# Kernel tuning notes

Hardware: AMD Instinct MI355X
Metric: run time of the kernel (lower is better)

Reference implementation:

```python
import jax, jax.numpy as jnp
import numpy as np

DIM = 512
HEADS = 8
HD = DIM // HEADS
WS = 4          # window_size
SHIFT = 2       # window_size // 2
HID = 4 * DIM   # mlp hidden
EPS = 1e-5


def _ln(x, g, b):
    m = jnp.mean(x, axis=-1, keepdims=True)
    v = jnp.mean((x - m) ** 2, axis=-1, keepdims=True)
    return (x - m) * jax.lax.rsqrt(v + EPS) * g + b


def setup_inputs() -> dict:
    key = jax.random.key(0)
    ks = jax.random.split(key, 12)
    s = 0.02
    return {
        "x": jax.random.normal(ks[0], (2, 32, 32, 32, DIM), dtype=jnp.float32),
        "ln1_g": jnp.ones((DIM,), jnp.float32),
        "ln1_b": jnp.zeros((DIM,), jnp.float32),
        "qkv_w": jax.random.normal(ks[1], (DIM, 3 * DIM), jnp.float32) * s,
        "qkv_b": jnp.zeros((3 * DIM,), jnp.float32),
        "proj_w": jax.random.normal(ks[2], (DIM, DIM), jnp.float32) * s,
        "proj_b": jnp.zeros((DIM,), jnp.float32),
        "ln2_g": jnp.ones((DIM,), jnp.float32),
        "ln2_b": jnp.zeros((DIM,), jnp.float32),
        "ffn_w1": jax.random.normal(ks[3], (DIM, HID), jnp.float32) * s,
        "ffn_b1": jnp.zeros((HID,), jnp.float32),
        "ffn_w2": jax.random.normal(ks[4], (HID, DIM), jnp.float32) * s,
        "ffn_b2": jnp.zeros((DIM,), jnp.float32),
    }


def reference(x, ln1_g, ln1_b, qkv_w, qkv_b, proj_w, proj_b,
              ln2_g, ln2_b, ffn_w1, ffn_b1, ffn_w2, ffn_b2):
    B, D, H, W, C = x.shape
    nD, nH, nW = D // WS, H // WS, W // WS
    N = WS ** 3

    # cyclic shift
    xs = jnp.roll(x, (-SHIFT, -SHIFT, -SHIFT), axis=(1, 2, 3))

    # window partition: (B*numWin, N, C)
    xw = xs.reshape(B, nD, WS, nH, WS, nW, WS, C)
    xw = xw.transpose(0, 1, 3, 5, 2, 4, 6, 7).reshape(-1, N, C)

    # pre-norm attention
    h = _ln(xw, ln1_g, ln1_b)
    qkv = (h @ qkv_w + qkv_b).reshape(-1, N, 3, HEADS, HD)
    q, k, v = jnp.moveaxis(qkv, 2, 0)          # each (Bn, N, HEADS, HD)
    scale = HD ** -0.5
    logits = jnp.einsum('bnhd,bmhd->bhnm', q, k) * scale
    attn = jax.nn.softmax(logits, axis=-1)
    out = jnp.einsum('bhnm,bmhd->bnhd', attn, v).reshape(-1, N, C)
    out = out @ proj_w + proj_b
    xw = xw + out

    # window reverse + unshift
    xo = xw.reshape(B, nD, nH, nW, WS, WS, WS, C)
    xo = xo.transpose(0, 1, 4, 2, 5, 3, 6, 7).reshape(B, D, H, W, C)
    xo = jnp.roll(xo, (SHIFT, SHIFT, SHIFT), axis=(1, 2, 3))

    # pre-norm FFN (exact GELU, dropout inactive in eval)
    h2 = _ln(xo, ln2_g, ln2_b)
    ffn = jax.nn.gelu(h2 @ ffn_w1 + ffn_b1, approximate=False) @ ffn_w2 + ffn_b2
    return xo + ffn
```

## Files before the change

### kernel.cpp

```cpp
#include <hip/hip_runtime.h>
#include <hip/hip_bf16.h>


typedef __attribute__((ext_vector_type(4))) short short4v;
typedef __attribute__((ext_vector_type(8))) short short8v;
typedef __attribute__((ext_vector_type(4))) float f32x4;

__device__ __forceinline__ unsigned short f2bf(float f) {
  unsigned u = __float_as_uint(f);
  u += 0x7fffu + ((u >> 16) & 1u);
  return (unsigned short)(u >> 16);
}

__device__ __forceinline__ float erf_fast(float x) {
  float ax = fabsf(x);
  float y = 1.0f + 0.3275911f * ax;
  float t;
  asm("v_rcp_f32 %0, %1" : "=v"(t) : "v"(y));
  float p = t * (0.254829592f +
            t * (-0.284496736f +
            t * (1.421413741f +
            t * (-1.453152027f +
            t * 1.061405429f))));
  float e = __expf(-ax * ax);
  float r = 1.0f - p * e;
  return copysignf(r, x);
}

__device__ __forceinline__ void gload_lds16(const unsigned short* g, unsigned short* l) {
  __builtin_amdgcn_global_load_lds(
      (const __attribute__((address_space(1))) unsigned int*)g,
      (__attribute__((address_space(3))) unsigned int*)l, 16, 0, 0);
}

__global__ __launch_bounds__(256)
void wprep_all(const float* __restrict__ qkv_w, const float* __restrict__ proj_w,
               const float* __restrict__ w1, const float* __restrict__ w2,
               unsigned short* __restrict__ wt) {
  int idx = blockIdx.x * 256 + threadIdx.x;
  const float* w; int kbits, N, base;
  if (idx < 786432)       { w = qkv_w;  kbits = 9;  N = 1536; base = 0; }
  else if (idx < 1048576) { w = proj_w; kbits = 9;  N = 512;  base = 786432; }
  else if (idx < 2097152) { w = w1;     kbits = 9;  N = 2048; base = 1048576; }
  else                    { w = w2;     kbits = 11; N = 512;  base = 2097152; }
  int li = idx - base;
  int K = 1 << kbits;
  int n = li >> kbits, kk = li & (K - 1);
  wt[idx] = f2bf(w[(long)kk * N + n]);
}

__global__ __launch_bounds__(256)
void ln_kernel(const float* __restrict__ src, const float* __restrict__ g,
               const float* __restrict__ bb, unsigned short* __restrict__ dst,
               const int gather) {
  const int lane = threadIdx.x & 63;
  const int row = blockIdx.x * 4 + (threadIdx.x >> 6);
  long srow;
  if (gather) {
    int n = row & 63, win = row >> 6;
    int w0 = win & 7, h0 = (win >> 3) & 7, d0 = (win >> 6) & 7, b2 = win >> 9;
    int dx = n & 3, dy = (n >> 2) & 3, dz = n >> 4;
    int od = (d0 * 4 + dz + 2) & 31, oh = (h0 * 4 + dy + 2) & 31, ow = (w0 * 4 + dx + 2) & 31;
    srow = (((long)b2 * 32 + od) * 32 + oh) * 32 + ow;
  } else {
    srow = row;
  }
  const float4* sp = (const float4*)(src + srow * 512);
  float4 x0 = sp[lane], x1 = sp[lane + 64];
  float sum = x0.x + x0.y + x0.z + x0.w + x1.x + x1.y + x1.z + x1.w;
  float sq  = x0.x*x0.x + x0.y*x0.y + x0.z*x0.z + x0.w*x0.w
            + x1.x*x1.x + x1.y*x1.y + x1.z*x1.z + x1.w*x1.w;
#pragma unroll
  for (int off = 1; off < 64; off <<= 1) {
    sum += __shfl_xor(sum, off, 64);
    sq  += __shfl_xor(sq, off, 64);
  }
  float mean = sum * (1.0f / 512.0f);
  float var  = sq * (1.0f / 512.0f) - mean * mean;
  float rstd = rsqrtf(var + 1e-5f);
  float4 g0 = ((const float4*)g)[lane], g1 = ((const float4*)g)[lane + 64];
  float4 b0 = ((const float4*)bb)[lane], b1v = ((const float4*)bb)[lane + 64];
  ushort4 o0, o1;
  o0.x = f2bf((x0.x - mean) * rstd * g0.x + b0.x);
  o0.y = f2bf((x0.y - mean) * rstd * g0.y + b0.y);
  o0.z = f2bf((x0.z - mean) * rstd * g0.z + b0.z);
  o0.w = f2bf((x0.w - mean) * rstd * g0.w + b0.w);
  o1.x = f2bf((x1.x - mean) * rstd * g1.x + b1v.x);
  o1.y = f2bf((x1.y - mean) * rstd * g1.y + b1v.y);
  o1.z = f2bf((x1.z - mean) * rstd * g1.z + b1v.z);
  o1.w = f2bf((x1.w - mean) * rstd * g1.w + b1v.w);
  *(ushort4*)(dst + (long)row * 512 + lane * 4) = o0;
  *(ushort4*)(dst + (long)row * 512 + 256 + lane * 4) = o1;
}

template <int EPI>
__global__ __launch_bounds__(512, 2)
void gemm_bt(const unsigned short* __restrict__ A,
             const unsigned short* __restrict__ Bt,
             const float* __restrict__ bias, int K,
             void* __restrict__ out0,
             unsigned short* __restrict__ out1,
             unsigned short* __restrict__ out2,
             const float* __restrict__ res) {
  __shared__ unsigned short SB[4][2][8192];
  const int tid = threadIdx.x;
  const int lane = tid & 63;
  const int wv = tid >> 6;
  const int wm = wv >> 2;
  const int wn = wv & 3;
  const int quad = lane >> 4;
  const int l15 = lane & 15;

  const int gx = gridDim.x;
  const int nwg = gx * gridDim.y;
  const int bid = blockIdx.y * gx + blockIdx.x;
  const int cpx = nwg >> 3;
  const int wg2 = (bid & 7) * cpx + (bid >> 3);
  const int bx = wg2 % gx;
  const int by = wg2 / gx;
  const long row0 = (long)by * 256;
  const long col0 = (long)bx * 256;

  f32x4 acc[8][4] = {};

  const int srow = wv * 16 + (lane >> 2);
  const int scg  = (lane & 3) ^ ((lane >> 3) & 3);
  const unsigned short* gA0 = A  + (row0 + srow) * K + scg * 8;
  const unsigned short* gB0 = Bt + (col0 + srow) * K + scg * 8;
  const long j1 = 128L * K;
  const int lds0 = srow * 32 + (lane & 3) * 8;

#define STAGE(v) do {                                              \
    const int q_ = (v) & 3; const long ko_ = (long)(v) * 32;       \
    gload_lds16(gA0 + ko_,      &SB[q_][0][lds0]);                 \
    gload_lds16(gA0 + ko_ + j1, &SB[q_][0][lds0 + 4096]);          \
    gload_lds16(gB0 + ko_,      &SB[q_][1][lds0]);                 \
    gload_lds16(gB0 + ko_ + j1, &SB[q_][1][lds0 + 4096]);          \
  } while (0)

  const int slot = (quad ^ ((l15 >> 1) & 3)) * 8;
  const int aoff = (wm * 128 + l15) * 32 + slot;
  const int boff = (wn * 64  + l15) * 32 + slot;

  const int nsub = K >> 5;
  STAGE(0); STAGE(1); STAGE(2);

  for (int u = 0; u < nsub; ++u) {
    if (u < nsub - 2)       asm volatile("s_waitcnt vmcnt(8)" ::: "memory");
    else if (u == nsub - 2) asm volatile("s_waitcnt vmcnt(4)" ::: "memory");
    else                    asm volatile("s_waitcnt vmcnt(0)" ::: "memory");
    __builtin_amdgcn_s_barrier();
    __builtin_amdgcn_sched_barrier(0);
    if (u + 3 < nsub) STAGE(u + 3);

    const unsigned short* Au = &SB[u & 3][0][0];
    const unsigned short* Bu = &SB[u & 3][1][0];
    short8v bf[4];
#pragma unroll
    for (int nt = 0; nt < 4; ++nt) bf[nt] = *(const short8v*)&Bu[boff + nt * 512];
#pragma unroll
    for (int mh = 0; mh < 2; ++mh) {
      short8v af[4];
#pragma unroll
      for (int i = 0; i < 4; ++i) af[i] = *(const short8v*)&Au[aoff + (mh * 4 + i) * 512];
      __builtin_amdgcn_s_setprio(1);
#pragma unroll
      for (int i = 0; i < 4; ++i)
#pragma unroll
        for (int nt = 0; nt < 4; ++nt)
          acc[mh * 4 + i][nt] = __builtin_amdgcn_mfma_f32_16x16x32_bf16(
              af[i], bf[nt], acc[mh * 4 + i][nt], 0, 0, 0);
      __builtin_amdgcn_s_setprio(0);
    }
    __builtin_amdgcn_sched_barrier(0);
  }
#undef STAGE

#pragma unroll
  for (int mt = 0; mt < 8; ++mt) {
#pragma unroll
    for (int nt = 0; nt < 4; ++nt) {
#pragma unroll
      for (int r = 0; r < 4; ++r) {
        const long gr = row0 + wm * 128 + mt * 16 + quad * 4 + r;
        const long gc = col0 + wn * 64 + nt * 16 + l15;
        float val = acc[mt][nt][r] + bias[gc];
        if (EPI == 0) {
          int which = (int)(gc >> 9), rem = (int)gc & 511;
          int head = rem >> 6, hd = rem & 63;
          long win = gr >> 6, n = gr & 63;
          long base = (win * 8 + head) * 4096;
          unsigned short bv = f2bf(val);
          if (which == 0)      ((unsigned short*)out0)[base + n * 64 + hd] = bv;
          else if (which == 1) out1[base + n * 64 + hd] = bv;
          else                 out2[base + hd * 64 + n] = bv;
        } else if (EPI == 1) {
          int win = (int)(gr >> 6), n = (int)gr & 63;
          int w0 = win & 7, h0 = (win >> 3) & 7, d0 = (win >> 6) & 7, b2 = win >> 9;
          int dx = n & 3, dy = (n >> 2) & 3, dz = n >> 4;
          int od = (d0 * 4 + dz + 2) & 31, oh = (h0 * 4 + dy + 2) & 31, ow = (w0 * 4 + dx + 2) & 31;
          long addr = ((((long)b2 * 32 + od) * 32 + oh) * 32 + ow) * 512 + gc;
          ((float*)out0)[addr] = res[addr] + val;
        } else if (EPI == 2) {
          float ge = 0.5f * val * (1.0f + erf_fast(val * 0.70710678118654752f));
          ((unsigned short*)out0)[gr * 2048 + gc] = f2bf(ge);
        } else {
          long addr = gr * 512 + gc;
          ((float*)out0)[addr] = res[addr] + val;
        }
      }
    }
  }
}

__global__ __launch_bounds__(256)
void attn_kernel(const unsigned short* __restrict__ q,
                 const unsigned short* __restrict__ k,
                 const unsigned short* __restrict__ vt,
                 unsigned short* __restrict__ out) {
  __shared__ unsigned short Ps[4][64 * 72];
  const int lane = threadIdx.x & 63;
  const int wave = threadIdx.x >> 6;
  const int quad = lane >> 4;
  const int l15 = lane & 15;
  const int unit = blockIdx.x * 4 + wave;
  const int win = unit >> 3;
  const int head = unit & 7;
  const long base = (long)unit * 4096;

  f32x4 s[4][4] = {};
#pragma unroll
  for (int kk = 0; kk < 64; kk += 32) {
    short8v a[4], b[4];
#pragma unroll
    for (int t = 0; t < 4; ++t) {
      a[t] = *(const short8v*)(q + base + (t * 16 + l15) * 64 + kk + quad * 8);
      b[t] = *(const short8v*)(k + base + (t * 16 + l15) * 64 + kk + quad * 8);
    }
#pragma unroll
    for (int mt = 0; mt < 4; ++mt)
#pragma unroll
      for (int nt = 0; nt < 4; ++nt)
        s[mt][nt] = __builtin_amdgcn_mfma_f32_16x16x32_bf16(a[mt], b[nt], s[mt][nt], 0, 0, 0);
  }

  float lrow[4][4];
#pragma unroll
  for (int mt = 0; mt < 4; ++mt) {
#pragma unroll
    for (int r = 0; r < 4; ++r) {
      float v0 = s[mt][0][r] * 0.125f, v1 = s[mt][1][r] * 0.125f;
      float v2 = s[mt][2][r] * 0.125f, v3 = s[mt][3][r] * 0.125f;
      float mx = fmaxf(fmaxf(v0, v1), fmaxf(v2, v3));
#pragma unroll
      for (int off = 1; off < 16; off <<= 1) mx = fmaxf(mx, __shfl_xor(mx, off, 64));
      v0 = __expf(v0 - mx); v1 = __expf(v1 - mx);
      v2 = __expf(v2 - mx); v3 = __expf(v3 - mx);
      float sm = v0 + v1 + v2 + v3;
#pragma unroll
      for (int off = 1; off < 16; off <<= 1) sm += __shfl_xor(sm, off, 64);
      lrow[mt][r] = sm;
      int row = mt * 16 + quad * 4 + r;
      Ps[wave][row * 72 + 0 + l15]  = f2bf(v0);
      Ps[wave][row * 72 + 16 + l15] = f2bf(v1);
      Ps[wave][row * 72 + 32 + l15] = f2bf(v2);
      Ps[wave][row * 72 + 48 + l15] = f2bf(v3);
    }
  }
  __syncthreads();

  f32x4 o[4][4] = {};
#pragma unroll
  for (int kk = 0; kk < 64; kk += 32) {
    short8v a[4], b[4];
#pragma unroll
    for (int t = 0; t < 4; ++t) {
      a[t] = *(const short8v*)(&Ps[wave][(t * 16 + l15) * 72 + kk + quad * 8]);
      b[t] = *(const short8v*)(vt + base + (t * 16 + l15) * 64 + kk + quad * 8);
    }
#pragma unroll
    for (int mt = 0; mt < 4; ++mt)
#pragma unroll
      for (int nt = 0; nt < 4; ++nt)
        o[mt][nt] = __builtin_amdgcn_mfma_f32_16x16x32_bf16(a[mt], b[nt], o[mt][nt], 0, 0, 0);
  }

#pragma unroll
  for (int mt = 0; mt < 4; ++mt)
#pragma unroll
    for (int nt = 0; nt < 4; ++nt)
#pragma unroll
      for (int r = 0; r < 4; ++r) {
        int row = mt * 16 + quad * 4 + r;
        int col = nt * 16 + l15;
        float val = o[mt][nt][r] / lrow[mt][r];
        out[((long)win * 64 + row) * 512 + head * 64 + col] = f2bf(val);
      }
}

extern "C" void kernel_launch(void* const* d_in, const int* in_sizes, int n_in,
                              void* d_out, int out_size, void* d_ws, size_t ws_size,
                              hipStream_t stream) {
  const float* x      = (const float*)d_in[0];
  const float* ln1_g  = (const float*)d_in[1];
  const float* ln1_b  = (const float*)d_in[2];
  const float* qkv_w  = (const float*)d_in[3];
  const float* qkv_b  = (const float*)d_in[4];
  const float* proj_w = (const float*)d_in[5];
  const float* proj_b = (const float*)d_in[6];
  const float* ln2_g  = (const float*)d_in[7];
  const float* ln2_b  = (const float*)d_in[8];
  const float* w1     = (const float*)d_in[9];
  const float* b1     = (const float*)d_in[10];
  const float* w2     = (const float*)d_in[11];
  const float* b2     = (const float*)d_in[12];

  char* ws = (char*)d_ws;
  unsigned short* wt_all  = (unsigned short*)ws;
  unsigned short* wt_qkv  = (unsigned short*)(ws + 0);
  unsigned short* wt_proj = (unsigned short*)(ws + 1572864);
  unsigned short* wt_1    = (unsigned short*)(ws + 2097152);
  unsigned short* wt_2    = (unsigned short*)(ws + 4194304);
  float*          xo      = (float*)(ws + 8388608);
  unsigned short* h       = (unsigned short*)(ws + 142606336);
  unsigned short* attno   = (unsigned short*)(ws + 209715200);
  unsigned short* qb      = (unsigned short*)(ws + 276824064);
  unsigned short* kb      = (unsigned short*)(ws + 343932928);
  unsigned short* vb      = (unsigned short*)(ws + 411041792);
  unsigned short* hid     = (unsigned short*)(ws + 209715200);
  float* out = (float*)d_out;

  wprep_all<<<12288, 256, 0, stream>>>(qkv_w, proj_w, w1, w2, wt_all);

  ln_kernel<<<16384, 256, 0, stream>>>(x, ln1_g, ln1_b, h, 1);
  gemm_bt<0><<<dim3(6, 256), 512, 0, stream>>>(h, wt_qkv, qkv_b, 512, qb, kb, vb, nullptr);
  attn_kernel<<<2048, 256, 0, stream>>>(qb, kb, vb, attno);
  gemm_bt<1><<<dim3(2, 256), 512, 0, stream>>>(attno, wt_proj, proj_b, 512, xo, nullptr, nullptr, x);
  ln_kernel<<<16384, 256, 0, stream>>>(xo, ln2_g, ln2_b, h, 0);
  gemm_bt<2><<<dim3(8, 256), 512, 0, stream>>>(h, wt_1, b1, 512, hid, nullptr, nullptr, nullptr);
  gemm_bt<3><<<dim3(2, 256), 512, 0, stream>>>(hid, wt_2, b2, 2048, out, nullptr, nullptr, xo);
}
```

Before: 1.071 ms.

## Fuse projection GEMM with residual and LayerNorm; stage QKV epilogue through LDS

Adds a gemm_ln kernel in which each block computes a full 128x512 row tile of the projection GEMM. It adds bias and the residual, reduces row mean and variance across waves through shared memory, and writes both xo and the LN2 bf16 output, which removes the separate ln_kernel launch and its re-read of xo. The QKV GEMM epilogue now stages per-head tiles in LDS (transposed for V) and writes them out with coalesced 16-byte stores instead of scattered 2-byte writes. The fused kernel uses a single-pass sum and sum-of-squares variance, which is less numerically robust, and it launches only 512 blocks, which may limit occupancy.

```diff
diff --git a/kernel.cpp b/kernel.cpp
--- a/kernel.cpp
+++ b/kernel.cpp
@@ -176,6 +176,57 @@
   }
 #undef STAGE
 
+  if (EPI == 0) {
+    const int which = (int)(col0 >> 9);
+    const int head0 = ((int)col0 & 511) >> 6;
+    const int win0  = (int)(row0 >> 6);
+    unsigned short* OUT = (which == 0) ? (unsigned short*)out0
+                        : (which == 1) ? out1 : out2;
+    unsigned short* SBu = &SB[0][0][0];
+    __syncthreads();
+    if (which < 2) {
+#pragma unroll
+      for (int mt = 0; mt < 8; ++mt) {
+        const int grl = wm * 128 + mt * 16 + quad * 4;
+#pragma unroll
+        for (int nt = 0; nt < 4; ++nt) {
+          const int col = nt * 16 + l15;
+          const float bv = bias[col0 + wn * 64 + col];
+#pragma unroll
+          for (int r = 0; r < 4; ++r) {
+            const int row = grl + r;
+            SBu[((row >> 6) * 4 + wn) * 4096 + (row & 63) * 64 + col] =
+                f2bf(acc[mt][nt][r] + bv);
+          }
+        }
+      }
+    } else {
+#pragma unroll
+      for (int mt = 0; mt < 8; ++mt) {
+        const int grl = wm * 128 + mt * 16 + quad * 4;
+#pragma unroll
+        for (int nt = 0; nt < 4; ++nt) {
+          const int col = nt * 16 + l15;
+          const float bv = bias[col0 + wn * 64 + col];
+          ushort4 pk;
+          pk.x = f2bf(acc[mt][nt][0] + bv);
+          pk.y = f2bf(acc[mt][nt][1] + bv);
+          pk.z = f2bf(acc[mt][nt][2] + bv);
+          pk.w = f2bf(acc[mt][nt][3] + bv);
+          *(ushort4*)&SBu[((grl >> 6) * 4 + wn) * 4096 + col * 64 + (grl & 63)] = pk;
+        }
+      }
+    }
+    __syncthreads();
+#pragma unroll
+    for (int it = 0; it < 16; ++it) {
+      unsigned short* dst = OUT +
+          ((long)((win0 + (it >> 2)) * 8 + head0 + (it & 3))) * 4096 + tid * 8;
+      *(short8v*)dst = *(const short8v*)&SBu[it * 4096 + tid * 8];
+    }
+    return;
+  }
+
 #pragma unroll
   for (int mt = 0; mt < 8; ++mt) {
 #pragma unroll
@@ -185,29 +236,144 @@
         const long gr = row0 + wm * 128 + mt * 16 + quad * 4 + r;
         const long gc = col0 + wn * 64 + nt * 16 + l15;
         float val = acc[mt][nt][r] + bias[gc];
-        if (EPI == 0) {
-          int which = (int)(gc >> 9), rem = (int)gc & 511;
-          int head = rem >> 6, hd = rem & 63;
-          long win = gr >> 6, n = gr & 63;
-          long base = (win * 8 + head) * 4096;
-          unsigned short bv = f2bf(val);
-          if (which == 0)      ((unsigned short*)out0)[base + n * 64 + hd] = bv;
-          else if (which == 1) out1[base + n * 64 + hd] = bv;
-          else                 out2[base + hd * 64 + n] = bv;
-        } else if (EPI == 1) {
-          int win = (int)(gr >> 6), n = (int)gr & 63;
-          int w0 = win & 7, h0 = (win >> 3) & 7, d0 = (win >> 6) & 7, b2 = win >> 9;
-          int dx = n & 3, dy = (n >> 2) & 3, dz = n >> 4;
-          int od = (d0 * 4 + dz + 2) & 31, oh = (h0 * 4 + dy + 2) & 31, ow = (w0 * 4 + dx + 2) & 31;
-          long addr = ((((long)b2 * 32 + od) * 32 + oh) * 32 + ow) * 512 + gc;
-          ((float*)out0)[addr] = res[addr] + val;
-        } else if (EPI == 2) {
+        if (EPI == 2) {
           float ge = 0.5f * val * (1.0f + erf_fast(val * 0.70710678118654752f));
           ((unsigned short*)out0)[gr * 2048 + gc] = f2bf(ge);
         } else {
           long addr = gr * 512 + gc;
           ((float*)out0)[addr] = res[addr] + val;
         }
+      }
+    }
+  }
+}
+
+__global__ __launch_bounds__(512, 2)
+void gemm_ln(const unsigned short* __restrict__ A,
+             const unsigned short* __restrict__ Bt,
+             const float* __restrict__ bias,
+             const float* __restrict__ res,
+             const float* __restrict__ g2, const float* __restrict__ b2v,
+             float* __restrict__ xo, unsigned short* __restrict__ h2) {
+  __shared__ unsigned short SB[3][20480];
+  const int tid = threadIdx.x;
+  const int lane = tid & 63;
+  const int wv = tid >> 6;
+  const int wm = wv >> 2;
+  const int wn = wv & 3;
+  const int quad = lane >> 4;
+  const int l15 = lane & 15;
+
+  const int bid = blockIdx.x;
+  const int by = (bid & 7) * 64 + (bid >> 3);
+  const long row0 = (long)by * 128;
+
+  f32x4 acc[4][8] = {};
+
+  const int srow = wv * 16 + (lane >> 2);
+  const int scg  = (lane & 3) ^ ((lane >> 3) & 3);
+  const unsigned short* gA0 = A  + (row0 + srow) * 512 + scg * 8;
+  const unsigned short* gB0 = Bt + srow * 512 + scg * 8;
+  const int lds0 = srow * 32 + (lane & 3) * 8;
+
+#define STAGEL(v) do {                                             \
+    unsigned short* s_ = &SB[(v) % 3][0];                          \
+    const long ko_ = (long)(v) * 32;                               \
+    gload_lds16(gA0 + ko_,               &s_[lds0]);               \
+    gload_lds16(gB0 + ko_,               &s_[4096  + lds0]);       \
+    gload_lds16(gB0 + ko_ + 128L * 512,  &s_[8192  + lds0]);       \
+    gload_lds16(gB0 + ko_ + 256L * 512,  &s_[12288 + lds0]);       \
+    gload_lds16(gB0 + ko_ + 384L * 512,  &s_[16384 + lds0]);       \
+  } while (0)
+
+  const int slot = (quad ^ ((l15 >> 1) & 3)) * 8;
+  const int aoff = (wm * 64 + l15) * 32 + slot;
+  const int boff = 4096 + (wn * 128 + l15) * 32 + slot;
+
+  STAGEL(0); STAGEL(1);
+
+  for (int u = 0; u < 16; ++u) {
+    if (u < 15) asm volatile("s_waitcnt vmcnt(5)" ::: "memory");
+    else        asm volatile("s_waitcnt vmcnt(0)" ::: "memory");
+    __builtin_amdgcn_s_barrier();
+    __builtin_amdgcn_sched_barrier(0);
+    if (u + 2 < 16) STAGEL(u + 2);
+
+    const unsigned short* Su = &SB[u % 3][0];
+    short8v af[4], bf[8];
+#pragma unroll
+    for (int i = 0; i < 4; ++i)  af[i] = *(const short8v*)&Su[aoff + i * 512];
+#pragma unroll
+    for (int nt = 0; nt < 8; ++nt) bf[nt] = *(const short8v*)&Su[boff + nt * 512];
+    __builtin_amdgcn_s_setprio(1);
+#pragma unroll
+    for (int i = 0; i < 4; ++i)
+#pragma unroll
+      for (int nt = 0; nt < 8; ++nt)
+        acc[i][nt] = __builtin_amdgcn_mfma_f32_16x16x32_bf16(
+            af[i], bf[nt], acc[i][nt], 0, 0, 0);
+    __builtin_amdgcn_s_setprio(0);
+    __builtin_amdgcn_sched_barrier(0);
+  }
+#undef STAGEL
+
+  __syncthreads();
+  float* part = (float*)&SB[0][0];
+
+#pragma unroll
+  for (int mt = 0; mt < 4; ++mt) {
+#pragma unroll
+    for (int r = 0; r < 4; ++r) {
+      const int gr = (int)row0 + wm * 64 + mt * 16 + quad * 4 + r;
+      const int win = gr >> 6, n = gr & 63;
+      const int w0 = win & 7, h0 = (win >> 3) & 7, d0 = (win >> 6) & 7, b2i = win >> 9;
+      const int dx = n & 3, dy = (n >> 2) & 3, dz = n >> 4;
+      const int od = (d0 * 4 + dz + 2) & 31, oh = (h0 * 4 + dy + 2) & 31, ow = (w0 * 4 + dx + 2) & 31;
+      const long sp = (((long)b2i * 32 + od) * 32 + oh) * 32 + ow;
+      float s = 0.f, q = 0.f;
+#pragma unroll
+      for (int nt = 0; nt < 8; ++nt) {
+        const int gc = wn * 128 + nt * 16 + l15;
+        float v = acc[mt][nt][r] + bias[gc] + res[sp * 512 + gc];
+        acc[mt][nt][r] = v;
+        s += v; q += v * v;
+      }
+#pragma unroll
+      for (int off = 1; off < 16; off <<= 1) {
+        s += __shfl_xor(s, off, 64);
+        q += __shfl_xor(q, off, 64);
+      }
+      if (l15 == 0) {
+        const int rowl = wm * 64 + mt * 16 + quad * 4 + r;
+        *(float2*)&part[(rowl * 4 + wn) * 2] = make_float2(s, q);
+      }
+    }
+  }
+  __syncthreads();
+
+#pragma unroll
+  for (int mt = 0; mt < 4; ++mt) {
+#pragma unroll
+    for (int r = 0; r < 4; ++r) {
+      const int rowl = wm * 64 + mt * 16 + quad * 4 + r;
+      const float4 p0 = *(const float4*)&part[rowl * 8];
+      const float4 p1 = *(const float4*)&part[rowl * 8 + 4];
+      const float s = p0.x + p0.z + p1.x + p1.z;
+      const float q = p0.y + p0.w + p1.y + p1.w;
+      const float mean = s * (1.0f / 512.0f);
+      const float rstd = rsqrtf(q * (1.0f / 512.0f) - mean * mean + 1e-5f);
+      const int gr = (int)row0 + rowl;
+      const int win = gr >> 6, n = gr & 63;
+      const int w0 = win & 7, h0 = (win >> 3) & 7, d0 = (win >> 6) & 7, b2i = win >> 9;
+      const int dx = n & 3, dy = (n >> 2) & 3, dz = n >> 4;
+      const int od = (d0 * 4 + dz + 2) & 31, oh = (h0 * 4 + dy + 2) & 31, ow = (w0 * 4 + dx + 2) & 31;
+      const long sp = (((long)b2i * 32 + od) * 32 + oh) * 32 + ow;
+#pragma unroll
+      for (int nt = 0; nt < 8; ++nt) {
+        const int gc = wn * 128 + nt * 16 + l15;
+        const float v = acc[mt][nt][r];
+        xo[sp * 512 + gc] = v;
+        h2[sp * 512 + gc] = f2bf((v - mean) * rstd * g2[gc] + b2v[gc]);
       }
     }
   }
@@ -335,8 +501,7 @@
   ln_kernel<<<16384, 256, 0, stream>>>(x, ln1_g, ln1_b, h, 1);
   gemm_bt<0><<<dim3(6, 256), 512, 0, stream>>>(h, wt_qkv, qkv_b, 512, qb, kb, vb, nullptr);
   attn_kernel<<<2048, 256, 0, stream>>>(qb, kb, vb, attno);
-  gemm_bt<1><<<dim3(2, 256), 512, 0, stream>>>(attno, wt_proj, proj_b, 512, xo, nullptr, nullptr, x);
-  ln_kernel<<<16384, 256, 0, stream>>>(xo, ln2_g, ln2_b, h, 0);
+  gemm_ln<<<512, 512, 0, stream>>>(attno, wt_proj, proj_b, x, ln2_g, ln2_b, xo, h);
   gemm_bt<2><<<dim3(8, 256), 512, 0, stream>>>(h, wt_1, b1, 512, hid, nullptr, nullptr, nullptr);
   gemm_bt<3><<<dim3(2, 256), 512, 0, stream>>>(hid, wt_2, b2, 2048, out, nullptr, nullptr, xo);
 }
```

Measured after the change: 985.4 us. -8.0%, faster.
